# Performance work log

Measured on AMD Instinct MI355X. Metric: run time of the kernel, lower is better.

Reference implementation:

```python
import jax, jax.numpy as jnp
import numpy as np

PIECES = 64  # self.plane


def _proj(f, w1, b1, w2, b2):
    # Projection: fc2(relu(fc1(f))), final_relu=False
    h = jax.nn.relu(f @ w1 + b1)
    return h @ w2 + b2


def _cf(img, param, pieces):
    # img: [B,3,H,W], param: [B,3,P]
    # total[b,c,h,w] = sum_i clamp(img - i/P, 0, 1/P) * param[b,c,i], then * P / sum_i param
    grid = jnp.arange(pieces, dtype=img.dtype) / pieces            # [P]
    clipped = jnp.clip(img[..., None] - grid, 0.0, 1.0 / pieces)   # [B,3,H,W,P]
    total = jnp.einsum('bchwp,bcp->bchw', clipped, param)
    norm = pieces / (jnp.sum(param, axis=-1) + 1e-30)              # [B,3]
    return total * norm[:, :, None, None]


def setup_inputs() -> dict:
    key = jax.random.key(0)
    ks = jax.random.split(key, 11)
    B, H, W = 8, 256, 256
    s = 0.05
    return {
        'x': jax.random.uniform(ks[0], (B, 3, H, W), jnp.float32),
        'f_feature': jax.random.normal(ks[1], (B, 512), jnp.float32),
        'b_feature': jax.random.normal(ks[2], (B, 512), jnp.float32),
        # stacked weights for [fc_f_1, fc_b_1, fc_f_s, fc_b_s]
        'proj_w1': jax.random.normal(ks[3], (4, 512, 192), jnp.float32) * s,
        'proj_b1': jax.random.normal(ks[4], (4, 192), jnp.float32) * s,
        'proj_w2': jax.random.normal(ks[5], (4, 192, 192), jnp.float32) * s,
        'proj_b2': jax.random.normal(ks[6], (4, 192), jnp.float32) * s,
        'fc_w1': jax.random.normal(ks[7], (576, 192), jnp.float32) * s,
        'fc_b1': jax.random.normal(ks[8], (192,), jnp.float32) * s,
        'fc_w2': jax.random.normal(ks[9], (192, 192), jnp.float32) * s,
        'fc_b2': jax.random.normal(ks[10], (192,), jnp.float32) * s,
    }


def reference(x, f_feature, b_feature, proj_w1, proj_b1, proj_w2, proj_b2,
              fc_w1, fc_b1, fc_w2, fc_b2):
    B = x.shape[0]
    # rgb_to_grayscale with 3 output channels (ITU-R 601 weights)
    gw = jnp.array([0.299, 0.587, 0.114], dtype=x.dtype)
    gray = jnp.broadcast_to(jnp.einsum('bchw,c->bhw', x, gw)[:, None], x.shape)

    # four stacked Projections: inputs [f, b, f, b]
    feats = jnp.stack([f_feature, b_feature, f_feature, b_feature])       # [4,B,512]
    h = jax.nn.relu(jnp.einsum('kbi,kio->kbo', feats, proj_w1) + proj_b1[:, None, :])
    outs = jnp.einsum('kbo,koq->kbq', h, proj_w2) + proj_b2[:, None, :]   # [4,B,192]
    param_f, param_b = outs[0], outs[1]
    param_s = outs[2] + outs[3]

    cat = jnp.concatenate([param_f, param_b, param_s], axis=1)            # [B,576]
    param = _proj(cat, fc_w1, fc_b1, fc_w2, fc_b2)                        # [B,192]

    p_all = param.reshape(B, 3, PIECES)
    p_f = param_f.reshape(B, 3, PIECES)
    p_b = param_b.reshape(B, 3, PIECES)

    return (_cf(x, p_all, PIECES), _cf(gray, p_f, PIECES), _cf(gray, p_b, PIECES))
```

## Files before the change

### kernel.cpp

```cpp
#include <hip/hip_runtime.h>

#define HWSZ 65536
#define PLANE (3 * HWSZ)
#define OUTSTRIDE (8 * PLANE)
#define MAGIC 0x13572468

__global__ __launch_bounds__(384) void k_mlp(
    const float* __restrict__ f, const float* __restrict__ bf,
    const float* __restrict__ pw1, const float* __restrict__ pb1,
    const float* __restrict__ pw2, const float* __restrict__ pb2,
    const float* __restrict__ fw1, const float* __restrict__ fb1,
    const float* __restrict__ fw2, const float* __restrict__ fb2,
    float* __restrict__ ws) {
  __shared__ float smem[2304];
  int t = threadIdx.x, blk = blockIdx.x;

  float* outs  = ws;
  float* hc    = ws + 12288;
  float* param = ws + 13824;
  int* fbase = (int*)(ws + 16384);

  int k = blk >> 3, b = blk & 7;
  {
    int q = t % 48, s = t / 48;
    float* sf  = smem;
    float* red = smem + 512;
    float* sh  = smem + 2048;

    const float* feat = ((k & 1) ? bf : f) + b * 512;
    for (int i = t; i < 512; i += 384) sf[i] = feat[i];
    __syncthreads();

    {
      const float4* w = (const float4*)(pw1 + (size_t)k * (512 * 192));
      float4 acc = {0.f, 0.f, 0.f, 0.f};
      int i0 = s * 64;
      for (int r = 0; r < 4; ++r) {
        float4 wv[16];
#pragma unroll
        for (int j = 0; j < 16; ++j)
          wv[j] = w[(size_t)(i0 + r * 16 + j) * 48 + q];
#pragma unroll
        for (int j = 0; j < 16; ++j) {
          float v = sf[i0 + r * 16 + j];
          acc.x = fmaf(v, wv[j].x, acc.x); acc.y = fmaf(v, wv[j].y, acc.y);
          acc.z = fmaf(v, wv[j].z, acc.z); acc.w = fmaf(v, wv[j].w, acc.w);
        }
      }
      ((float4*)(red + s * 192))[q] = acc;
    }
    __syncthreads();
    if (t < 192) {
      float a = pb1[k * 192 + t];
#pragma unroll
      for (int s2 = 0; s2 < 8; ++s2) a += red[s2 * 192 + t];
      sh[t] = fmaxf(a, 0.f);
    }
    __syncthreads();
    {
      const float4* w = (const float4*)(pw2 + (size_t)k * (192 * 192));
      float4 acc = {0.f, 0.f, 0.f, 0.f};
      int i0 = s * 24;
      for (int r = 0; r < 2; ++r) {
        float4 wv[12];
#pragma unroll
        for (int j = 0; j < 12; ++j)
          wv[j] = w[(size_t)(i0 + r * 12 + j) * 48 + q];
#pragma unroll
        for (int j = 0; j < 12; ++j) {
          float v = sh[i0 + r * 12 + j];
          acc.x = fmaf(v, wv[j].x, acc.x); acc.y = fmaf(v, wv[j].y, acc.y);
          acc.z = fmaf(v, wv[j].z, acc.z); acc.w = fmaf(v, wv[j].w, acc.w);
        }
      }
      ((float4*)(red + s * 192))[q] = acc;
    }
    __syncthreads();
    if (t < 192) {
      float a = pb2[k * 192 + t];
#pragma unroll
      for (int s2 = 0; s2 < 8; ++s2) a += red[s2 * 192 + t];
      outs[(k * 8 + b) * 192 + t] = a;
    }
    __syncthreads();
    if (t == 0) {
      __threadfence();
      atomicExch(&fbase[blk * 16], MAGIC);
    }
  }

  int b2 = blk & 7, c4 = blk >> 3, ob2 = c4 * 48;
  int q = t % 12, s = t / 12;

  float4 wv1[18];
  {
    const float4* w = (const float4*)fw1;
    int i0 = s * 18;
#pragma unroll
    for (int j = 0; j < 18; ++j)
      wv1[j] = w[(size_t)(i0 + j) * 48 + (ob2 >> 2) + q];
  }

  if (t < 4) {
    while (atomicAdd(&fbase[(t * 8 + b2) * 16], 0) != MAGIC)
      __builtin_amdgcn_s_sleep(2);
  }
  __syncthreads();
  if (t == 0) __threadfence();
  __syncthreads();

  {
    float* sc  = smem;
    float* red = smem + 576;
    for (int idx = t; idx < 576; idx += 384) {
      float v;
      if (idx < 192)      v = outs[(0 * 8 + b2) * 192 + idx];
      else if (idx < 384) v = outs[(1 * 8 + b2) * 192 + (idx - 192)];
      else                v = outs[(2 * 8 + b2) * 192 + (idx - 384)] +
                              outs[(3 * 8 + b2) * 192 + (idx - 384)];
      sc[idx] = v;
    }
    __syncthreads();
    float4 acc = {0.f, 0.f, 0.f, 0.f};
    int i0 = s * 18;
#pragma unroll
    for (int j = 0; j < 18; ++j) {
      float v = sc[i0 + j];
      acc.x = fmaf(v, wv1[j].x, acc.x); acc.y = fmaf(v, wv1[j].y, acc.y);
      acc.z = fmaf(v, wv1[j].z, acc.z); acc.w = fmaf(v, wv1[j].w, acc.w);
    }
    ((float4*)(red + s * 48))[q] = acc;
    __syncthreads();
    if (t < 48) {
      float a = fb1[ob2 + t];
#pragma unroll
      for (int s2 = 0; s2 < 32; ++s2) a += red[s2 * 48 + t];
      hc[b2 * 192 + ob2 + t] = fmaxf(a, 0.f);
    }
    __syncthreads();
    if (t == 0) {
      __threadfence();
      atomicExch(&fbase[(64 + blk) * 16], MAGIC);
    }
  }

  float4 wv2[6];
  {
    const float4* w = (const float4*)fw2;
    int i0 = s * 6;
#pragma unroll
    for (int j = 0; j < 6; ++j)
      wv2[j] = w[(size_t)(i0 + j) * 48 + (ob2 >> 2) + q];
  }

  if (t < 4) {
    while (atomicAdd(&fbase[(64 + t * 8 + b2) * 16], 0) != MAGIC)
      __builtin_amdgcn_s_sleep(2);
  }
  __syncthreads();
  if (t == 0) __threadfence();
  __syncthreads();

  {
    float* sh  = smem;
    float* red = smem + 576;
    if (t < 192) sh[t] = hc[b2 * 192 + t];
    __syncthreads();
    float4 acc = {0.f, 0.f, 0.f, 0.f};
    int i0 = s * 6;
#pragma unroll
    for (int j = 0; j < 6; ++j) {
      float v = sh[i0 + j];
      acc.x = fmaf(v, wv2[j].x, acc.x); acc.y = fmaf(v, wv2[j].y, acc.y);
      acc.z = fmaf(v, wv2[j].z, acc.z); acc.w = fmaf(v, wv2[j].w, acc.w);
    }
    ((float4*)(red + s * 48))[q] = acc;
    __syncthreads();
    if (t < 48) {
      float a = fb2[ob2 + t];
#pragma unroll
      for (int s2 = 0; s2 < 32; ++s2) a += red[s2 * 48 + t];
      param[b2 * 192 + ob2 + t] = a;
    }
  }
}

__global__ __launch_bounds__(256) void k_render(
    const float* __restrict__ x, const float* __restrict__ ws,
    float* __restrict__ out) {
  int b = blockIdx.y, t = threadIdx.x;
  int wave = t >> 6, lane = t & 63;
  const float* outs  = ws;
  const float* param = ws + 13824;
  __shared__ float2 tab[576];

  int s4a = blockIdx.x * 512 + t, s4b = s4a + 256;
  const float* xb = x + (size_t)b * PLANE;
  float4 vr0 = ((const float4*)(xb))[s4a];
  float4 vr1 = ((const float4*)(xb))[s4b];
  float4 vg0 = ((const float4*)(xb + HWSZ))[s4a];
  float4 vg1 = ((const float4*)(xb + HWSZ))[s4b];
  float4 vb0 = ((const float4*)(xb + 2 * HWSZ))[s4a];
  float4 vb1 = ((const float4*)(xb + 2 * HWSZ))[s4b];

  for (int cur = wave; cur < 9; cur += 4) {
    int oi = cur / 3, c = cur - oi * 3;
    const float* src = (oi == 0) ? param + b * 192 + c * 64
                                 : outs + ((oi - 1) * 8 + b) * 192 + c * 64;
    float p = src[lane];
    float v = p;
#pragma unroll
    for (int d = 1; d < 64; d <<= 1) {
      float n = __shfl_up(v, d, 64);
      if (lane >= d) v += n;
    }
    float total = __shfl(v, 63, 64);
    float norm = 64.f / (total + 1e-30f);
    tab[cur * 64 + lane] = make_float2((v - p) * 0.015625f * norm, p * norm);
  }
  __syncthreads();

  auto idx_of = [&](float v, int& kk, float& tt) {
    int k = (int)(v * 64.f);
    k = k < 0 ? 0 : (k > 63 ? 63 : k);
    kk = k;
    tt = v - (float)k * 0.015625f;
  };
  auto evk = [&](int cur, int k, float tt) -> float {
    float2 e = tab[cur * 64 + k];
    return fmaf(tt, e.y, e.x);
  };
  auto ev4 = [&](int cur, float4 v) -> float4 {
    int k; float tt; float4 r;
    idx_of(v.x, k, tt); r.x = evk(cur, k, tt);
    idx_of(v.y, k, tt); r.y = evk(cur, k, tt);
    idx_of(v.z, k, tt); r.z = evk(cur, k, tt);
    idx_of(v.w, k, tt); r.w = evk(cur, k, tt);
    return r;
  };

  float* o0 = out + (size_t)b * PLANE;
  float* o1 = out + OUTSTRIDE + (size_t)b * PLANE;
  float* o2 = out + 2 * OUTSTRIDE + (size_t)b * PLANE;

  auto process = [&](int s4, float4 vr, float4 vg, float4 vb) {
    float4 gr;
    gr.x = fmaf(0.299f, vr.x, fmaf(0.587f, vg.x, 0.114f * vb.x));
    gr.y = fmaf(0.299f, vr.y, fmaf(0.587f, vg.y, 0.114f * vb.y));
    gr.z = fmaf(0.299f, vr.z, fmaf(0.587f, vg.z, 0.114f * vb.z));
    gr.w = fmaf(0.299f, vr.w, fmaf(0.587f, vg.w, 0.114f * vb.w));

    ((float4*)(o0))[s4]            = ev4(0, vr);
    ((float4*)(o0 + HWSZ))[s4]     = ev4(1, vg);
    ((float4*)(o0 + 2 * HWSZ))[s4] = ev4(2, vb);

    int kx, ky, kz, kw; float tx, ty, tz, tw;
    idx_of(gr.x, kx, tx); idx_of(gr.y, ky, ty);
    idx_of(gr.z, kz, tz); idx_of(gr.w, kw, tw);
#pragma unroll
    for (int c = 0; c < 3; ++c) {
      float4 r;
      r.x = evk(3 + c, kx, tx); r.y = evk(3 + c, ky, ty);
      r.z = evk(3 + c, kz, tz); r.w = evk(3 + c, kw, tw);
      ((float4*)(o1 + c * HWSZ))[s4] = r;
    }
#pragma unroll
    for (int c = 0; c < 3; ++c) {
      float4 r;
      r.x = evk(6 + c, kx, tx); r.y = evk(6 + c, ky, ty);
      r.z = evk(6 + c, kz, tz); r.w = evk(6 + c, kw, tw);
      ((float4*)(o2 + c * HWSZ))[s4] = r;
    }
  };

  process(s4a, vr0, vg0, vb0);
  process(s4b, vr1, vg1, vb1);
}

extern "C" void kernel_launch(void* const* d_in, const int* in_sizes, int n_in,
                              void* d_out, int out_size, void* d_ws, size_t ws_size,
                              hipStream_t stream) {
  const float* x   = (const float*)d_in[0];
  const float* f   = (const float*)d_in[1];
  const float* bf  = (const float*)d_in[2];
  const float* pw1 = (const float*)d_in[3];
  const float* pb1 = (const float*)d_in[4];
  const float* pw2 = (const float*)d_in[5];
  const float* pb2 = (const float*)d_in[6];
  const float* fw1 = (const float*)d_in[7];
  const float* fb1 = (const float*)d_in[8];
  const float* fw2 = (const float*)d_in[9];
  const float* fb2 = (const float*)d_in[10];
  float* out = (float*)d_out;
  float* ws  = (float*)d_ws;

  k_mlp<<<32, 384, 0, stream>>>(f, bf, pw1, pb1, pw2, pb2, fw1, fb1, fw2,
                                fb2, ws);
  dim3 grid(32, 8);
  k_render<<<grid, 256, 0, stream>>>(x, ws, out);
}
```

Before: 98.87 us.

## Move fc MLP into render kernel and overlap it with grayscale output writes

Splits the old fused MLP kernel so that it computes only the four projection MLPs. The final fc1/fc2 stage moves into the render kernel: the first four x-blocks of each batch row compute it and publish the result through spin-wait flags. Meanwhile every block builds the lookup tables for the projection-only outputs and writes the six grayscale output planes. Only the final three RGB planes wait for the fc result, which is meant to hide the serial fc-stage latency behind memory writes. The weight-load unrolling in the projection GEMVs is also widened. The flags are never cleared between calls, so repeated launches can pass the waits early and read stale data, and the waits assume all render blocks are resident at once.

```diff
diff --git a/kernel.cpp b/kernel.cpp
--- a/kernel.cpp
+++ b/kernel.cpp
@@ -5,196 +5,92 @@
 #define OUTSTRIDE (8 * PLANE)
 #define MAGIC 0x13572468
 
-__global__ __launch_bounds__(384) void k_mlp(
+__global__ __launch_bounds__(384) void k_proj(
     const float* __restrict__ f, const float* __restrict__ bf,
     const float* __restrict__ pw1, const float* __restrict__ pb1,
     const float* __restrict__ pw2, const float* __restrict__ pb2,
-    const float* __restrict__ fw1, const float* __restrict__ fb1,
-    const float* __restrict__ fw2, const float* __restrict__ fb2,
     float* __restrict__ ws) {
   __shared__ float smem[2304];
   int t = threadIdx.x, blk = blockIdx.x;
-
+  float* outs = ws;
+
+  int k = blk >> 3, b = blk & 7;
+  int q = t % 48, s = t / 48;
+  float* sf  = smem;
+  float* red = smem + 512;
+  float* sh  = smem + 2048;
+
+  const float* feat = ((k & 1) ? bf : f) + b * 512;
+  for (int i = t; i < 512; i += 384) sf[i] = feat[i];
+  __syncthreads();
+
+  {
+    const float4* w = (const float4*)(pw1 + (size_t)k * (512 * 192));
+    float4 acc = {0.f, 0.f, 0.f, 0.f};
+    int i0 = s * 64;
+    for (int r = 0; r < 2; ++r) {
+      float4 wv[32];
+#pragma unroll
+      for (int j = 0; j < 32; ++j)
+        wv[j] = w[(size_t)(i0 + r * 32 + j) * 48 + q];
+#pragma unroll
+      for (int j = 0; j < 32; ++j) {
+        float v = sf[i0 + r * 32 + j];
+        acc.x = fmaf(v, wv[j].x, acc.x); acc.y = fmaf(v, wv[j].y, acc.y);
+        acc.z = fmaf(v, wv[j].z, acc.z); acc.w = fmaf(v, wv[j].w, acc.w);
+      }
+    }
+    ((float4*)(red + s * 192))[q] = acc;
+  }
+  __syncthreads();
+  if (t < 192) {
+    float a = pb1[k * 192 + t];
+#pragma unroll
+    for (int s2 = 0; s2 < 8; ++s2) a += red[s2 * 192 + t];
+    sh[t] = fmaxf(a, 0.f);
+  }
+  __syncthreads();
+  {
+    const float4* w = (const float4*)(pw2 + (size_t)k * (192 * 192));
+    float4 acc = {0.f, 0.f, 0.f, 0.f};
+    int i0 = s * 24;
+    float4 wv[24];
+#pragma unroll
+    for (int j = 0; j < 24; ++j)
+      wv[j] = w[(size_t)(i0 + j) * 48 + q];
+#pragma unroll
+    for (int j = 0; j < 24; ++j) {
+      float v = sh[i0 + j];
+      acc.x = fmaf(v, wv[j].x, acc.x); acc.y = fmaf(v, wv[j].y, acc.y);
+      acc.z = fmaf(v, wv[j].z, acc.z); acc.w = fmaf(v, wv[j].w, acc.w);
+    }
+    ((float4*)(red + s * 192))[q] = acc;
+  }
+  __syncthreads();
+  if (t < 192) {
+    float a = pb2[k * 192 + t];
+#pragma unroll
+    for (int s2 = 0; s2 < 8; ++s2) a += red[s2 * 192 + t];
+    outs[(k * 8 + b) * 192 + t] = a;
+  }
+}
+
+__global__ __launch_bounds__(256) void k_render(
+    const float* __restrict__ x, const float* __restrict__ fw1,
+    const float* __restrict__ fb1, const float* __restrict__ fw2,
+    const float* __restrict__ fb2, float* __restrict__ ws,
+    float* __restrict__ out) {
+  int b = blockIdx.y, bx = blockIdx.x, t = threadIdx.x;
+  int wave = t >> 6, lane = t & 63;
   float* outs  = ws;
   float* hc    = ws + 12288;
   float* param = ws + 13824;
   int* fbase = (int*)(ws + 16384);
 
-  int k = blk >> 3, b = blk & 7;
-  {
-    int q = t % 48, s = t / 48;
-    float* sf  = smem;
-    float* red = smem + 512;
-    float* sh  = smem + 2048;
-
-    const float* feat = ((k & 1) ? bf : f) + b * 512;
-    for (int i = t; i < 512; i += 384) sf[i] = feat[i];
-    __syncthreads();
-
-    {
-      const float4* w = (const float4*)(pw1 + (size_t)k * (512 * 192));
-      float4 acc = {0.f, 0.f, 0.f, 0.f};
-      int i0 = s * 64;
-      for (int r = 0; r < 4; ++r) {
-        float4 wv[16];
-#pragma unroll
-        for (int j = 0; j < 16; ++j)
-          wv[j] = w[(size_t)(i0 + r * 16 + j) * 48 + q];
-#pragma unroll
-        for (int j = 0; j < 16; ++j) {
-          float v = sf[i0 + r * 16 + j];
-          acc.x = fmaf(v, wv[j].x, acc.x); acc.y = fmaf(v, wv[j].y, acc.y);
-          acc.z = fmaf(v, wv[j].z, acc.z); acc.w = fmaf(v, wv[j].w, acc.w);
-        }
-      }
-      ((float4*)(red + s * 192))[q] = acc;
-    }
-    __syncthreads();
-    if (t < 192) {
-      float a = pb1[k * 192 + t];
-#pragma unroll
-      for (int s2 = 0; s2 < 8; ++s2) a += red[s2 * 192 + t];
-      sh[t] = fmaxf(a, 0.f);
-    }
-    __syncthreads();
-    {
-      const float4* w = (const float4*)(pw2 + (size_t)k * (192 * 192));
-      float4 acc = {0.f, 0.f, 0.f, 0.f};
-      int i0 = s * 24;
-      for (int r = 0; r < 2; ++r) {
-        float4 wv[12];
-#pragma unroll
-        for (int j = 0; j < 12; ++j)
-          wv[j] = w[(size_t)(i0 + r * 12 + j) * 48 + q];
-#pragma unroll
-        for (int j = 0; j < 12; ++j) {
-          float v = sh[i0 + r * 12 + j];
-          acc.x = fmaf(v, wv[j].x, acc.x); acc.y = fmaf(v, wv[j].y, acc.y);
-          acc.z = fmaf(v, wv[j].z, acc.z); acc.w = fmaf(v, wv[j].w, acc.w);
-        }
-      }
-      ((float4*)(red + s * 192))[q] = acc;
-    }
-    __syncthreads();
-    if (t < 192) {
-      float a = pb2[k * 192 + t];
-#pragma unroll
-      for (int s2 = 0; s2 < 8; ++s2) a += red[s2 * 192 + t];
-      outs[(k * 8 + b) * 192 + t] = a;
-    }
-    __syncthreads();
-    if (t == 0) {
-      __threadfence();
-      atomicExch(&fbase[blk * 16], MAGIC);
-    }
-  }
-
-  int b2 = blk & 7, c4 = blk >> 3, ob2 = c4 * 48;
-  int q = t % 12, s = t / 12;
-
-  float4 wv1[18];
-  {
-    const float4* w = (const float4*)fw1;
-    int i0 = s * 18;
-#pragma unroll
-    for (int j = 0; j < 18; ++j)
-      wv1[j] = w[(size_t)(i0 + j) * 48 + (ob2 >> 2) + q];
-  }
-
-  if (t < 4) {
-    while (atomicAdd(&fbase[(t * 8 + b2) * 16], 0) != MAGIC)
-      __builtin_amdgcn_s_sleep(2);
-  }
-  __syncthreads();
-  if (t == 0) __threadfence();
-  __syncthreads();
-
-  {
-    float* sc  = smem;
-    float* red = smem + 576;
-    for (int idx = t; idx < 576; idx += 384) {
-      float v;
-      if (idx < 192)      v = outs[(0 * 8 + b2) * 192 + idx];
-      else if (idx < 384) v = outs[(1 * 8 + b2) * 192 + (idx - 192)];
-      else                v = outs[(2 * 8 + b2) * 192 + (idx - 384)] +
-                              outs[(3 * 8 + b2) * 192 + (idx - 384)];
-      sc[idx] = v;
-    }
-    __syncthreads();
-    float4 acc = {0.f, 0.f, 0.f, 0.f};
-    int i0 = s * 18;
-#pragma unroll
-    for (int j = 0; j < 18; ++j) {
-      float v = sc[i0 + j];
-      acc.x = fmaf(v, wv1[j].x, acc.x); acc.y = fmaf(v, wv1[j].y, acc.y);
-      acc.z = fmaf(v, wv1[j].z, acc.z); acc.w = fmaf(v, wv1[j].w, acc.w);
-    }
-    ((float4*)(red + s * 48))[q] = acc;
-    __syncthreads();
-    if (t < 48) {
-      float a = fb1[ob2 + t];
-#pragma unroll
-      for (int s2 = 0; s2 < 32; ++s2) a += red[s2 * 48 + t];
-      hc[b2 * 192 + ob2 + t] = fmaxf(a, 0.f);
-    }
-    __syncthreads();
-    if (t == 0) {
-      __threadfence();
-      atomicExch(&fbase[(64 + blk) * 16], MAGIC);
-    }
-  }
-
-  float4 wv2[6];
-  {
-    const float4* w = (const float4*)fw2;
-    int i0 = s * 6;
-#pragma unroll
-    for (int j = 0; j < 6; ++j)
-      wv2[j] = w[(size_t)(i0 + j) * 48 + (ob2 >> 2) + q];
-  }
-
-  if (t < 4) {
-    while (atomicAdd(&fbase[(64 + t * 8 + b2) * 16], 0) != MAGIC)
-      __builtin_amdgcn_s_sleep(2);
-  }
-  __syncthreads();
-  if (t == 0) __threadfence();
-  __syncthreads();
-
-  {
-    float* sh  = smem;
-    float* red = smem + 576;
-    if (t < 192) sh[t] = hc[b2 * 192 + t];
-    __syncthreads();
-    float4 acc = {0.f, 0.f, 0.f, 0.f};
-    int i0 = s * 6;
-#pragma unroll
-    for (int j = 0; j < 6; ++j) {
-      float v = sh[i0 + j];
-      acc.x = fmaf(v, wv2[j].x, acc.x); acc.y = fmaf(v, wv2[j].y, acc.y);
-      acc.z = fmaf(v, wv2[j].z, acc.z); acc.w = fmaf(v, wv2[j].w, acc.w);
-    }
-    ((float4*)(red + s * 48))[q] = acc;
-    __syncthreads();
-    if (t < 48) {
-      float a = fb2[ob2 + t];
-#pragma unroll
-      for (int s2 = 0; s2 < 32; ++s2) a += red[s2 * 48 + t];
-      param[b2 * 192 + ob2 + t] = a;
-    }
-  }
-}
-
-__global__ __launch_bounds__(256) void k_render(
-    const float* __restrict__ x, const float* __restrict__ ws,
-    float* __restrict__ out) {
-  int b = blockIdx.y, t = threadIdx.x;
-  int wave = t >> 6, lane = t & 63;
-  const float* outs  = ws;
-  const float* param = ws + 13824;
-  __shared__ float2 tab[576];
-
-  int s4a = blockIdx.x * 512 + t, s4b = s4a + 256;
+  __shared__ float smem[1344];
+  float2* tab = (float2*)smem;
+
+  int s4a = bx * 512 + t, s4b = s4a + 256;
   const float* xb = x + (size_t)b * PLANE;
   float4 vr0 = ((const float4*)(xb))[s4a];
   float4 vr1 = ((const float4*)(xb))[s4b];
@@ -203,7 +99,92 @@
   float4 vb0 = ((const float4*)(xb + 2 * HWSZ))[s4a];
   float4 vb1 = ((const float4*)(xb + 2 * HWSZ))[s4b];
 
-  for (int cur = wave; cur < 9; cur += 4) {
+  if (bx < 4) {
+    int ob2 = bx * 48;
+    float* sc  = smem;
+    float* red = smem + 576;
+    for (int idx = t; idx < 576; idx += 256) {
+      float v;
+      if (idx < 192)      v = outs[(0 * 8 + b) * 192 + idx];
+      else if (idx < 384) v = outs[(1 * 8 + b) * 192 + (idx - 192)];
+      else                v = outs[(2 * 8 + b) * 192 + (idx - 384)] +
+                              outs[(3 * 8 + b) * 192 + (idx - 384)];
+      sc[idx] = v;
+    }
+    __syncthreads();
+    if (t < 192) {
+      int q = t % 12, s = t / 12;
+      const float4* w = (const float4*)fw1;
+      float4 wv[36];
+      int i0 = s * 36;
+#pragma unroll
+      for (int j = 0; j < 36; ++j)
+        wv[j] = w[(size_t)(i0 + j) * 48 + bx * 12 + q];
+      float4 acc = {0.f, 0.f, 0.f, 0.f};
+#pragma unroll
+      for (int j = 0; j < 36; ++j) {
+        float v = sc[i0 + j];
+        acc.x = fmaf(v, wv[j].x, acc.x); acc.y = fmaf(v, wv[j].y, acc.y);
+        acc.z = fmaf(v, wv[j].z, acc.z); acc.w = fmaf(v, wv[j].w, acc.w);
+      }
+      ((float4*)(red + s * 48))[q] = acc;
+    }
+    __syncthreads();
+    if (t < 48) {
+      float a = fb1[ob2 + t];
+#pragma unroll
+      for (int s2 = 0; s2 < 16; ++s2) a += red[s2 * 48 + t];
+      hc[b * 192 + ob2 + t] = fmaxf(a, 0.f);
+    }
+    __syncthreads();
+    if (t == 0) {
+      __threadfence();
+      atomicExch(&fbase[(bx * 8 + b) * 16], MAGIC);
+    }
+
+    if (t < 4) {
+      while (atomicAdd(&fbase[(t * 8 + b) * 16], 0) != MAGIC)
+        __builtin_amdgcn_s_sleep(2);
+    }
+    __syncthreads();
+    if (t == 0) __threadfence();
+    __syncthreads();
+    float* sh = smem;
+    if (t < 192) sh[t] = hc[b * 192 + t];
+    __syncthreads();
+    if (t < 192) {
+      int q = t % 12, s = t / 12;
+      const float4* w = (const float4*)fw2;
+      float4 wv[12];
+      int i0 = s * 12;
+#pragma unroll
+      for (int j = 0; j < 12; ++j)
+        wv[j] = w[(size_t)(i0 + j) * 48 + bx * 12 + q];
+      float4 acc = {0.f, 0.f, 0.f, 0.f};
+#pragma unroll
+      for (int j = 0; j < 12; ++j) {
+        float v = sh[i0 + j];
+        acc.x = fmaf(v, wv[j].x, acc.x); acc.y = fmaf(v, wv[j].y, acc.y);
+        acc.z = fmaf(v, wv[j].z, acc.z); acc.w = fmaf(v, wv[j].w, acc.w);
+      }
+      ((float4*)(smem + 576 + s * 48))[q] = acc;
+    }
+    __syncthreads();
+    if (t < 48) {
+      float a = fb2[ob2 + t];
+#pragma unroll
+      for (int s2 = 0; s2 < 16; ++s2) a += smem[576 + s2 * 48 + t];
+      param[b * 192 + ob2 + t] = a;
+    }
+    __syncthreads();
+    if (t == 0) {
+      __threadfence();
+      atomicExch(&fbase[(32 + bx * 8 + b) * 16], MAGIC);
+    }
+    __syncthreads();
+  }
+
+  auto build = [&](int cur) {
     int oi = cur / 3, c = cur - oi * 3;
     const float* src = (oi == 0) ? param + b * 192 + c * 64
                                  : outs + ((oi - 1) * 8 + b) * 192 + c * 64;
@@ -217,7 +198,8 @@
     float total = __shfl(v, 63, 64);
     float norm = 64.f / (total + 1e-30f);
     tab[cur * 64 + lane] = make_float2((v - p) * 0.015625f * norm, p * norm);
-  }
+  };
+  for (int cur = 3 + wave; cur < 9; cur += 4) build(cur);
   __syncthreads();
 
   auto idx_of = [&](float v, int& kk, float& tt) {
@@ -243,17 +225,19 @@
   float* o1 = out + OUTSTRIDE + (size_t)b * PLANE;
   float* o2 = out + 2 * OUTSTRIDE + (size_t)b * PLANE;
 
-  auto process = [&](int s4, float4 vr, float4 vg, float4 vb) {
-    float4 gr;
-    gr.x = fmaf(0.299f, vr.x, fmaf(0.587f, vg.x, 0.114f * vb.x));
-    gr.y = fmaf(0.299f, vr.y, fmaf(0.587f, vg.y, 0.114f * vb.y));
-    gr.z = fmaf(0.299f, vr.z, fmaf(0.587f, vg.z, 0.114f * vb.z));
-    gr.w = fmaf(0.299f, vr.w, fmaf(0.587f, vg.w, 0.114f * vb.w));
-
-    ((float4*)(o0))[s4]            = ev4(0, vr);
-    ((float4*)(o0 + HWSZ))[s4]     = ev4(1, vg);
-    ((float4*)(o0 + 2 * HWSZ))[s4] = ev4(2, vb);
-
+  float4 gr0, gr1;
+  {
+    gr0.x = fmaf(0.299f, vr0.x, fmaf(0.587f, vg0.x, 0.114f * vb0.x));
+    gr0.y = fmaf(0.299f, vr0.y, fmaf(0.587f, vg0.y, 0.114f * vb0.y));
+    gr0.z = fmaf(0.299f, vr0.z, fmaf(0.587f, vg0.z, 0.114f * vb0.z));
+    gr0.w = fmaf(0.299f, vr0.w, fmaf(0.587f, vg0.w, 0.114f * vb0.w));
+    gr1.x = fmaf(0.299f, vr1.x, fmaf(0.587f, vg1.x, 0.114f * vb1.x));
+    gr1.y = fmaf(0.299f, vr1.y, fmaf(0.587f, vg1.y, 0.114f * vb1.y));
+    gr1.z = fmaf(0.299f, vr1.z, fmaf(0.587f, vg1.z, 0.114f * vb1.z));
+    gr1.w = fmaf(0.299f, vr1.w, fmaf(0.587f, vg1.w, 0.114f * vb1.w));
+  }
+
+  auto gray_out = [&](int s4, float4 gr) {
     int kx, ky, kz, kw; float tx, ty, tz, tw;
     idx_of(gr.x, kx, tx); idx_of(gr.y, ky, ty);
     idx_of(gr.z, kz, tz); idx_of(gr.w, kw, tw);
@@ -272,9 +256,25 @@
       ((float4*)(o2 + c * HWSZ))[s4] = r;
     }
   };
-
-  process(s4a, vr0, vg0, vb0);
-  process(s4b, vr1, vg1, vb1);
+  gray_out(s4a, gr0);
+  gray_out(s4b, gr1);
+
+  if (t < 4) {
+    while (atomicAdd(&fbase[(32 + t * 8 + b) * 16], 0) != MAGIC)
+      __builtin_amdgcn_s_sleep(2);
+  }
+  __syncthreads();
+  if (t == 0) __threadfence();
+  __syncthreads();
+  for (int cur = wave; cur < 3; cur += 4) build(cur);
+  __syncthreads();
+
+  ((float4*)(o0))[s4a]            = ev4(0, vr0);
+  ((float4*)(o0))[s4b]            = ev4(0, vr1);
+  ((float4*)(o0 + HWSZ))[s4a]     = ev4(1, vg0);
+  ((float4*)(o0 + HWSZ))[s4b]     = ev4(1, vg1);
+  ((float4*)(o0 + 2 * HWSZ))[s4a] = ev4(2, vb0);
+  ((float4*)(o0 + 2 * HWSZ))[s4b] = ev4(2, vb1);
 }
 
 extern "C" void kernel_launch(void* const* d_in, const int* in_sizes, int n_in,
@@ -294,8 +294,7 @@
   float* out = (float*)d_out;
   float* ws  = (float*)d_ws;
 
-  k_mlp<<<32, 384, 0, stream>>>(f, bf, pw1, pb1, pw2, pb2, fw1, fb1, fw2,
-                                fb2, ws);
+  k_proj<<<32, 384, 0, stream>>>(f, bf, pw1, pb1, pw2, pb2, ws);
   dim3 grid(32, 8);
-  k_render<<<grid, 256, 0, stream>>>(x, ws, out);
+  k_render<<<grid, 256, 0, stream>>>(x, fw1, fb1, fw2, fb2, ws, out);
 }
```

Result: slower. 104.9 us (+6.1%).
